# Kernel tuning notes

Hardware: AMD Instinct MI355X
Metric: run time of the kernel (lower is better)

## Reference

```python
import jax, jax.numpy as jnp
import numpy as np

F_DIMS = [16, 16, 16, 16]
F_SIZES = [16, 32, 64, 96]
HID = 128  # == 2*sum(F_DIMS)
IN_DIM = 3
OUT_DIM = 3
N = 524288
N_LAYERS = 3
N_VEC_LAYERS = 2


def sample_grid(grid, coords):
    """Trilinear grid_sample, align_corners=True, border padding.
    grid: (C, S, S, S) laid out (D, H, W); coords: (N, 3) as (x, y, z) in [-1, 1]
    where x indexes W, y indexes H, z indexes D (torch grid_sample convention).
    Returns (N, C)."""
    S = grid.shape[1]
    p = jnp.clip((coords + 1.0) * 0.5 * (S - 1), 0.0, S - 1.0)
    p0 = jnp.floor(p)
    w = p - p0
    i0 = p0.astype(jnp.int32)
    i1 = jnp.minimum(i0 + 1, S - 1)
    x0, y0, z0 = i0[:, 0], i0[:, 1], i0[:, 2]
    x1, y1, z1 = i1[:, 0], i1[:, 1], i1[:, 2]
    wx, wy, wz = w[:, 0], w[:, 1], w[:, 2]
    g = lambda z, y, x: grid[:, z, y, x]  # (C, N)
    c00 = g(z0, y0, x0) * (1 - wx) + g(z0, y0, x1) * wx
    c01 = g(z0, y1, x0) * (1 - wx) + g(z0, y1, x1) * wx
    c10 = g(z1, y0, x0) * (1 - wx) + g(z1, y0, x1) * wx
    c11 = g(z1, y1, x0) * (1 - wx) + g(z1, y1, x1) * wx
    c0 = c00 * (1 - wy) + c01 * wy
    c1 = c10 * (1 - wy) + c11 * wy
    return (c0 * (1 - wz) + c1 * wz).T  # (N, C)


def multi_level(grids, coords):
    feats = jnp.concatenate([sample_grid(g, coords) for g in grids], axis=1)
    return jax.nn.silu(feats)


def setup_inputs() -> dict:
    key = jax.random.key(0)
    ks = jax.random.split(key, 24)
    inp = {}
    inp['physical_coords'] = jax.random.normal(ks[0], (N, IN_DIM), jnp.float32)
    inp['net_coords'] = jax.random.uniform(ks[1], (N, IN_DIM), jnp.float32, -1.0, 1.0)
    inp['tau'] = jax.random.uniform(ks[2], (N, 1), jnp.float32)
    scale = 0.01
    for i, (fd, fs) in enumerate(zip(F_DIMS, F_SIZES)):
        inp[f'vec_g{i}'] = scale * jax.random.normal(ks[3 + i], (fd, fs, fs, fs), jnp.float32)
        inp[f'tau_g{i}'] = scale * jax.random.normal(ks[7 + i], (fd, fs, fs, fs), jnp.float32)
    sfd = sum(F_DIMS)  # 64

    def ffm_weight(k):
        rd = jax.random.uniform(k, (sfd, IN_DIM), jnp.float32, -1.0, 1.0)
        rd = rd / jnp.linalg.norm(rd, axis=1, keepdims=True)
        return jnp.linspace(0.5, 4.0, sfd)[:, None] * rd

    inp['vec_pe_w'] = ffm_weight(ks[11])
    inp['tau_pe_w'] = ffm_weight(ks[12])
    inp['tau_pe_b'] = jnp.zeros((sfd,), jnp.float32)
    inp['vec_scale_param'] = jnp.ones((1, HID), jnp.float32) * 0.01
    inp['vec_map_w'] = jax.random.normal(ks[13], (N_VEC_LAYERS, HID, HID), jnp.float32) / np.sqrt(HID)
    inp['tau_mlp_w'] = jax.random.normal(ks[14], (HID, HID), jnp.float32) / np.sqrt(HID)
    inp['vec_mlp_w'] = jax.random.normal(ks[15], (N_LAYERS, HID, HID), jnp.float32) / np.sqrt(HID)
    inp['tau_params'] = jnp.ones((N_LAYERS, 1, HID), jnp.float32) * 0.01
    inp['last_w'] = jax.random.normal(ks[16], (OUT_DIM, HID), jnp.float32) / np.sqrt(HID)
    return inp


def reference(physical_coords, net_coords, tau,
              vec_g0, vec_g1, vec_g2, vec_g3,
              tau_g0, tau_g1, tau_g2, tau_g3,
              vec_pe_w, tau_pe_w, tau_pe_b, vec_scale_param,
              vec_map_w, tau_mlp_w, vec_mlp_w, tau_params, last_w):
    # vector branch
    vec_grid_f = multi_level([vec_g0, vec_g1, vec_g2, vec_g3], net_coords)  # (N, 64)
    vec_ffm = jnp.sin(net_coords @ vec_pe_w.T)                               # (N, 64)
    vec_features = jnp.concatenate([vec_grid_f, vec_ffm], axis=1)           # (N, 128)
    for i in range(vec_map_w.shape[0]):
        vec_features = jax.nn.silu(vec_features @ vec_map_w[i].T)
    # tau branch
    tau_grid_f = multi_level([tau_g0, tau_g1, tau_g2, tau_g3], net_coords)
    tau_ffm = jnp.sin(net_coords @ tau_pe_w.T + tau_pe_b)
    tau_features = jnp.concatenate([tau_grid_f, tau_ffm], axis=1)           # (N, 128)
    # residual MLP stack
    out = jnp.tanh(tau * vec_scale_param * vec_features)
    for idx in range(vec_mlp_w.shape[0]):
        t_tau = jnp.tanh(tau * tau_params[idx])
        h = out @ vec_mlp_w[idx].T
        if idx == 0:
            h = h * (tau_features @ tau_mlp_w.T)
        out = out + t_tau * jax.nn.silu(h)
    return physical_coords + out @ last_w.T
```

## Files before the change

### kernel.cpp

```cpp
#include <hip/hip_runtime.h>
#include <hip/hip_bf16.h>

typedef unsigned short u16;
typedef unsigned int   u32;
typedef short bf16x8 __attribute__((ext_vector_type(8)));
typedef float f32x4  __attribute__((ext_vector_type(4)));

#define N_PTS   524288

#define WS_TAU   18939904
#define WS_MAP   37879808
#define WS_TMLP  37912576
#define WS_MLP   37928960
#define WS_TOTAL_BYTES (37978112ULL * 2ULL)

__device__ __forceinline__ void ldsfence() { __asm__ __volatile__("" ::: "memory"); }

__device__ __forceinline__ float b2f(u16 b) {
    u32 u = ((u32)b) << 16; float f; __builtin_memcpy(&f, &u, 4); return f;
}
__device__ __forceinline__ u16 f2b(float f) {
    u32 u; __builtin_memcpy(&u, &f, 4);
    u32 r = (u + 0x7FFFu + ((u >> 16) & 1u)) >> 16;
    return (u16)r;
}
__device__ __forceinline__ float frcp(float x) { return __builtin_amdgcn_rcpf(x); }
__device__ __forceinline__ float fsilu(float x) { return x * frcp(1.f + __expf(-x)); }
__device__ __forceinline__ float ftanh(float x) {
    float e = __expf(2.f * x);
    return 1.f - 2.f * frcp(e + 1.f);
}
__device__ __forceinline__ float fsin(float a) {
    return __builtin_amdgcn_sinf(a * 0.15915494309189535f);
}

__device__ __forceinline__ int aidx(int row, int ch) {
    return (row << 7) + ((((ch >> 3) ^ (row & 7))) << 3) + (ch & 7);
}

__device__ __forceinline__ void store4(u16* actw, int row, int ch,
                                       float v0, float v1, float v2, float v3) {
    u32 lo = (u32)f2b(v0) | ((u32)f2b(v1) << 16);
    u32 hi = (u32)f2b(v2) | ((u32)f2b(v3) << 16);
    *(uint2*)(actw + aidx(row, ch)) = make_uint2(lo, hi);
}

struct GridPtrs { const float* g[4]; };

struct PrepArgs {
    const float* vg[4]; const float* tg[4];
    const float* map_w; const float* tmlp; const float* mlp;
    u16* ws;
};
#define PREP_VOXB 9248
__global__ void __launch_bounds__(256) dtn_prep(PrepArgs p) {
    int b = blockIdx.x;
    if (b < PREP_VOXB) {
        int v = b * 256 + threadIdx.x;
        int set = (v >= 1183744) ? 1 : 0;
        int lv = v - set * 1183744;
        int l, base, S3, off;
        if      (lv <   4096) { l = 0; base = 0;      S3 = 4096;   off = 0;       }
        else if (lv <  36864) { l = 1; base = 4096;   S3 = 32768;  off = 65536;   }
        else if (lv < 299008) { l = 2; base = 36864;  S3 = 262144; off = 589824;  }
        else                  { l = 3; base = 299008; S3 = 884736; off = 4784128; }
        int vox = lv - base;
        const float* src = set ? p.tg[l] : p.vg[l];
        u16* dst = p.ws + (set ? WS_TAU : 0) + off + (size_t)vox * 16;
        u32 packed[8];
#pragma unroll
        for (int c = 0; c < 8; ++c) {
            u32 lo = f2b(src[(2 * c) * S3 + vox]);
            u32 hi = f2b(src[(2 * c + 1) * S3 + vox]);
            packed[c] = lo | (hi << 16);
        }
        uint4* d = (uint4*)dst;
        d[0] = make_uint4(packed[0], packed[1], packed[2], packed[3]);
        d[1] = make_uint4(packed[4], packed[5], packed[6], packed[7]);
    } else {
        int i = (b - PREP_VOXB) * 256 + threadIdx.x;
        if (i < 32768)      p.ws[WS_MAP  + i]          = f2b(p.map_w[i]);
        else if (i < 49152) p.ws[WS_TMLP + (i - 32768)] = f2b(p.tmlp[i - 32768]);
        else if (i < 98304) p.ws[WS_MLP  + (i - 49152)] = f2b(p.mlp[i - 49152]);
    }
}

template<int USE_WS, int HASB>
__device__ __forceinline__ void featurize(const u16* __restrict__ gT, GridPtrs gp,
                                          float x, float y, float z,
                                          const float* __restrict__ pe_w,
                                          const float* __restrict__ pe_b,
                                          u16* __restrict__ actw, int row)
{
    const int Ss[4]   = {16, 32, 64, 96};
    const int offs[4] = {0, 65536, 589824, 4784128};
    const int S3s[4]  = {4096, 32768, 262144, 884736};
#pragma unroll
    for (int l = 0; l < 4; ++l) {
        const int S = Ss[l];
        float fS = (float)(S - 1);
        float px = fminf(fmaxf((x + 1.f) * 0.5f * fS, 0.f), fS);
        float py = fminf(fmaxf((y + 1.f) * 0.5f * fS, 0.f), fS);
        float pz = fminf(fmaxf((z + 1.f) * 0.5f * fS, 0.f), fS);
        int ix0 = (int)px, iy0 = (int)py, iz0 = (int)pz;
        float wx = px - (float)ix0, wy = py - (float)iy0, wz = pz - (float)iz0;
        int ix1 = min(ix0 + 1, S - 1), iy1 = min(iy0 + 1, S - 1), iz1 = min(iz0 + 1, S - 1);

        float f[16];
#pragma unroll
        for (int c = 0; c < 16; ++c) f[c] = 0.f;

#pragma unroll
        for (int cz = 0; cz < 2; ++cz) {
            int zz = cz ? iz1 : iz0;
            float wgtz = cz ? wz : (1.f - wz);
#pragma unroll
            for (int cy = 0; cy < 2; ++cy) {
                int yy = cy ? iy1 : iy0;
                float wgty = wgtz * (cy ? wy : (1.f - wy));
#pragma unroll
                for (int cx = 0; cx < 2; ++cx) {
                    int xx = cx ? ix1 : ix0;
                    float wgt = wgty * (cx ? wx : (1.f - wx));
                    if (USE_WS) {
                        const u16* g = gT + offs[l];
                        const uint4* p = (const uint4*)(g + (size_t)(((zz * S) + yy) * S + xx) * 16);
                        uint4 a = p[0], b = p[1];
                        f[0]  += wgt * b2f((u16)(a.x & 0xffff));  f[1]  += wgt * b2f((u16)(a.x >> 16));
                        f[2]  += wgt * b2f((u16)(a.y & 0xffff));  f[3]  += wgt * b2f((u16)(a.y >> 16));
                        f[4]  += wgt * b2f((u16)(a.z & 0xffff));  f[5]  += wgt * b2f((u16)(a.z >> 16));
                        f[6]  += wgt * b2f((u16)(a.w & 0xffff));  f[7]  += wgt * b2f((u16)(a.w >> 16));
                        f[8]  += wgt * b2f((u16)(b.x & 0xffff));  f[9]  += wgt * b2f((u16)(b.x >> 16));
                        f[10] += wgt * b2f((u16)(b.y & 0xffff));  f[11] += wgt * b2f((u16)(b.y >> 16));
                        f[12] += wgt * b2f((u16)(b.z & 0xffff));  f[13] += wgt * b2f((u16)(b.z >> 16));
                        f[14] += wgt * b2f((u16)(b.w & 0xffff));  f[15] += wgt * b2f((u16)(b.w >> 16));
                    } else {
                        const float* gc = gp.g[l];
                        size_t vox = (size_t)((zz * S) + yy) * S + xx;
#pragma unroll
                        for (int c = 0; c < 16; ++c)
                            f[c] += wgt * gc[(size_t)c * S3s[l] + vox];
                    }
                }
            }
        }
#pragma unroll
        for (int c = 0; c < 16; c += 4)
            store4(actw, row, l * 16 + c,
                   fsilu(f[c]), fsilu(f[c + 1]), fsilu(f[c + 2]), fsilu(f[c + 3]));
    }
#pragma unroll 4
    for (int fc = 0; fc < 64; fc += 4) {
        float s[4];
#pragma unroll
        for (int j = 0; j < 4; ++j) {
            int ch = fc + j;
            float a = x * pe_w[ch * 3 + 0] + y * pe_w[ch * 3 + 1] + z * pe_w[ch * 3 + 2];
            if (HASB) a += pe_b[ch];
            s[j] = fsin(a);
        }
        store4(actw, row, 64 + fc, s[0], s[1], s[2], s[3]);
    }
}

__device__ __forceinline__ void loadB(const u16* actw, bf16x8 B[4][4], int l16, int quad) {
#pragma unroll
    for (int nt = 0; nt < 4; ++nt)
#pragma unroll
        for (int kt = 0; kt < 4; ++kt)
            B[nt][kt] = *(const bf16x8*)(actw + aidx(nt * 16 + l16, kt * 32 + quad * 8));
    ldsfence();
}

template<int USE_WS>
__device__ __forceinline__ bf16x8 loadA(const u16* WT, const float* Wf, int row, int chunk) {
    if (USE_WS) {
        return ((const bf16x8*)WT)[row * 16 + chunk];
    } else {
        const float4* p = (const float4*)(Wf + row * 128 + chunk * 8);
        float4 f0 = p[0], f1 = p[1];
        u32 w0 = (u32)f2b(f0.x) | ((u32)f2b(f0.y) << 16);
        u32 w1 = (u32)f2b(f0.z) | ((u32)f2b(f0.w) << 16);
        u32 w2 = (u32)f2b(f1.x) | ((u32)f2b(f1.y) << 16);
        u32 w3 = (u32)f2b(f1.z) | ((u32)f2b(f1.w) << 16);
        uint4 packed = make_uint4(w0, w1, w2, w3);
        bf16x8 r; __builtin_memcpy(&r, &packed, 16); return r;
    }
}

template<int USE_WS, typename Epi>
__device__ __forceinline__ void gemm128(const u16* __restrict__ WT, const float* __restrict__ Wf,
                                        const bf16x8 B[4][4],
                                        int l16, int quad, Epi&& epi)
{
#pragma unroll
    for (int mt = 0; mt < 8; ++mt) {
        f32x4 acc[4];
#pragma unroll
        for (int nt = 0; nt < 4; ++nt) acc[nt] = (f32x4){0.f, 0.f, 0.f, 0.f};
#pragma unroll
        for (int kt = 0; kt < 4; ++kt) {
            bf16x8 a = loadA<USE_WS>(WT, Wf, mt * 16 + l16, kt * 4 + quad);
#pragma unroll
            for (int nt = 0; nt < 4; ++nt)
                acc[nt] = __builtin_amdgcn_mfma_f32_16x16x32_bf16(a, B[nt][kt], acc[nt], 0, 0, 0);
        }
#pragma unroll
        for (int nt = 0; nt < 4; ++nt) epi(mt, nt, acc[nt]);
    }
}

template<int USE_WS>
__global__ void __launch_bounds__(64, 4)
dtn_main(const float* __restrict__ nc, const float* __restrict__ tauP,
         const float* __restrict__ phys, const u16* __restrict__ wsT,
         GridPtrs vgp, GridPtrs tgp,
         const float* __restrict__ vec_pe_w, const float* __restrict__ tau_pe_w,
         const float* __restrict__ tau_pe_b, const float* __restrict__ vscale,
         const float* __restrict__ map_w, const float* __restrict__ tau_mlp_w,
         const float* __restrict__ mlp_w, const float* __restrict__ tau_pars,
         const float* __restrict__ last_w, float* __restrict__ outP)
{
    __shared__ __align__(16) u16 actw[64 * 128];
    const int lane = threadIdx.x;
    const int quad = lane >> 4, l16 = lane & 15;

    const int pBase = blockIdx.x * 64;
    const int myPt  = pBase + lane;

    float cx = nc[myPt * 3 + 0];
    float cy = nc[myPt * 3 + 1];
    float cz = nc[myPt * 3 + 2];

    float tauv[4];
#pragma unroll
    for (int nt = 0; nt < 4; ++nt) tauv[nt] = tauP[pBase + nt * 16 + l16];

    const u16* wsVec = wsT;
    const u16* wsTau = wsT + WS_TAU;
    const u16* wMap  = wsT + WS_MAP;
    const u16* wTmlp = wsT + WS_TMLP;
    const u16* wMlp  = wsT + WS_MLP;

    featurize<USE_WS, 1>(wsTau, tgp, cx, cy, cz, tau_pe_w, tau_pe_b, actw, lane);
    __syncthreads();

    bf16x8 B[4][4];
    loadB(actw, B, l16, quad);
    u32 tfpPk[64];
    gemm128<USE_WS>(wTmlp, tau_mlp_w, B, l16, quad, [&](int mt, int nt, f32x4 acc) {
        int base = (mt * 4 + nt) * 2;
        tfpPk[base + 0] = (u32)f2b(acc[0]) | ((u32)f2b(acc[1]) << 16);
        tfpPk[base + 1] = (u32)f2b(acc[2]) | ((u32)f2b(acc[3]) << 16);
    });
    __syncthreads();

    featurize<USE_WS, 0>(wsVec, vgp, cx, cy, cz, vec_pe_w, (const float*)nullptr, actw, lane);
    __syncthreads();

    loadB(actw, B, l16, quad);
    gemm128<USE_WS>(wMap, map_w, B, l16, quad, [&](int mt, int nt, f32x4 acc) {
        int cb = mt * 16 + quad * 4, pt = nt * 16 + l16;
        store4(actw, pt, cb, fsilu(acc[0]), fsilu(acc[1]), fsilu(acc[2]), fsilu(acc[3]));
    });
    __syncthreads();

    loadB(actw, B, l16, quad);
    gemm128<USE_WS>(wMap + 128 * 128, map_w + 128 * 128, B, l16, quad, [&](int mt, int nt, f32x4 acc) {
        int cb = mt * 16 + quad * 4, pt = nt * 16 + l16;
        float t = tauv[nt];
        float4 vs = *(const float4*)(vscale + cb);
        store4(actw, pt, cb,
               ftanh(t * vs.x * fsilu(acc[0])), ftanh(t * vs.y * fsilu(acc[1])),
               ftanh(t * vs.z * fsilu(acc[2])), ftanh(t * vs.w * fsilu(acc[3])));
    });
    __syncthreads();

#pragma unroll
    for (int idx = 0; idx < 3; ++idx) {
        loadB(actw, B, l16, quad);
        gemm128<USE_WS>(wMlp + idx * 128 * 128, mlp_w + idx * 128 * 128, B, l16, quad,
                        [&](int mt, int nt, f32x4 acc) {
            int cb = mt * 16 + quad * 4, pt = nt * 16 + l16;
            float t = tauv[nt];
            float4 tp = *(const float4*)(tau_pars + idx * 128 + cb);
            uint2 old = *(const uint2*)(actw + aidx(pt, cb));
            float h0 = acc[0], h1 = acc[1], h2 = acc[2], h3 = acc[3];
            if (idx == 0) {
                int base = (mt * 4 + nt) * 2;
                h0 *= b2f((u16)(tfpPk[base] & 0xffff));
                h1 *= b2f((u16)(tfpPk[base] >> 16));
                h2 *= b2f((u16)(tfpPk[base + 1] & 0xffff));
                h3 *= b2f((u16)(tfpPk[base + 1] >> 16));
            }
            float n0 = b2f((u16)(old.x & 0xffff)) + ftanh(t * tp.x) * fsilu(h0);
            float n1 = b2f((u16)(old.x >> 16))    + ftanh(t * tp.y) * fsilu(h1);
            float n2 = b2f((u16)(old.y & 0xffff)) + ftanh(t * tp.z) * fsilu(h2);
            float n3 = b2f((u16)(old.y >> 16))    + ftanh(t * tp.w) * fsilu(h3);
            store4(actw, pt, cb, n0, n1, n2, n3);
        });
        __syncthreads();
    }

    float a0 = 0.f, a1 = 0.f, a2 = 0.f;
#pragma unroll
    for (int c8 = 0; c8 < 16; ++c8) {
        bf16x8 v = *(const bf16x8*)(actw + aidx(lane, c8 * 8));
        const u16* vp = (const u16*)&v;
#pragma unroll
        for (int j = 0; j < 8; ++j) {
            float av = b2f(vp[j]);
            int k = c8 * 8 + j;
            a0 += av * last_w[0 * 128 + k];
            a1 += av * last_w[1 * 128 + k];
            a2 += av * last_w[2 * 128 + k];
        }
    }
    outP[myPt * 3 + 0] = phys[myPt * 3 + 0] + a0;
    outP[myPt * 3 + 1] = phys[myPt * 3 + 1] + a1;
    outP[myPt * 3 + 2] = phys[myPt * 3 + 2] + a2;
}

extern "C" void kernel_launch(void* const* d_in, const int* in_sizes, int n_in,
                              void* d_out, int out_size, void* d_ws, size_t ws_size,
                              hipStream_t stream)
{
    const float* phys     = (const float*)d_in[0];
    const float* nc       = (const float*)d_in[1];
    const float* tau      = (const float*)d_in[2];
    GridPtrs vgp, tgp;
    bool interleaved = (in_sizes[4] == 65536);
    for (int l = 0; l < 4; ++l) {
        if (interleaved) {
            vgp.g[l] = (const float*)d_in[3 + 2 * l];
            tgp.g[l] = (const float*)d_in[4 + 2 * l];
        } else {
            vgp.g[l] = (const float*)d_in[3 + l];
            tgp.g[l] = (const float*)d_in[7 + l];
        }
    }
    const float* vec_pe_w = (const float*)d_in[11];
    const float* tau_pe_w = (const float*)d_in[12];
    const float* tau_pe_b = (const float*)d_in[13];
    const float* vscale   = (const float*)d_in[14];
    const float* map_w    = (const float*)d_in[15];
    const float* tau_mlp  = (const float*)d_in[16];
    const float* mlp_w    = (const float*)d_in[17];
    const float* tau_pars = (const float*)d_in[18];
    const float* last_w   = (const float*)d_in[19];
    u16* wsT = (u16*)d_ws;

    bool useWs = (ws_size >= WS_TOTAL_BYTES);
    if (useWs) {
        PrepArgs pa;
        for (int l = 0; l < 4; ++l) { pa.vg[l] = vgp.g[l]; pa.tg[l] = tgp.g[l]; }
        pa.map_w = map_w; pa.tmlp = tau_mlp; pa.mlp = mlp_w; pa.ws = wsT;
        dtn_prep<<<PREP_VOXB + 384, 256, 0, stream>>>(pa);
        dtn_main<1><<<N_PTS / 64, 64, 0, stream>>>(nc, tau, phys, wsT, vgp, tgp,
                                                   vec_pe_w, tau_pe_w, tau_pe_b, vscale,
                                                   map_w, tau_mlp, mlp_w, tau_pars, last_w,
                                                   (float*)d_out);
    } else {
        dtn_main<0><<<N_PTS / 64, 64, 0, stream>>>(nc, tau, phys, wsT, vgp, tgp,
                                                   vec_pe_w, tau_pe_w, tau_pe_b, vscale,
                                                   map_w, tau_mlp, mlp_w, tau_pars, last_w,
                                                   (float*)d_out);
    }
}
```

Measured before the change: 832.8 us.

## Split each 64-point block across four waves for featurize and GEMM work

The main kernel goes from one 64-thread wave per 64-point block to four waves. In featurization each wave handles one grid level and its 16 Fourier channels for all 64 points. In the GEMMs each wave owns 16 rows (points) and keeps only one N-tile of B fragments and accumulators. The last projection is split across quads and reduced with lane shuffles. The aim is to cut per-thread register pressure and serial latency by raising wave-level parallelism, at the cost of more block-level syncs and redundant weight A-fragment loads per wave.

```diff
diff --git a/kernel.cpp b/kernel.cpp
--- a/kernel.cpp
+++ b/kernel.cpp
@@ -85,72 +85,81 @@
     }
 }
 
-template<int USE_WS, int HASB>
-__device__ __forceinline__ void featurize(const u16* __restrict__ gT, GridPtrs gp,
-                                          float x, float y, float z,
-                                          const float* __restrict__ pe_w,
-                                          const float* __restrict__ pe_b,
-                                          u16* __restrict__ actw, int row)
-{
-    const int Ss[4]   = {16, 32, 64, 96};
-    const int offs[4] = {0, 65536, 589824, 4784128};
-    const int S3s[4]  = {4096, 32768, 262144, 884736};
-#pragma unroll
-    for (int l = 0; l < 4; ++l) {
-        const int S = Ss[l];
-        float fS = (float)(S - 1);
-        float px = fminf(fmaxf((x + 1.f) * 0.5f * fS, 0.f), fS);
-        float py = fminf(fmaxf((y + 1.f) * 0.5f * fS, 0.f), fS);
-        float pz = fminf(fmaxf((z + 1.f) * 0.5f * fS, 0.f), fS);
-        int ix0 = (int)px, iy0 = (int)py, iz0 = (int)pz;
-        float wx = px - (float)ix0, wy = py - (float)iy0, wz = pz - (float)iz0;
-        int ix1 = min(ix0 + 1, S - 1), iy1 = min(iy0 + 1, S - 1), iz1 = min(iz0 + 1, S - 1);
-
-        float f[16];
-#pragma unroll
-        for (int c = 0; c < 16; ++c) f[c] = 0.f;
-
-#pragma unroll
-        for (int cz = 0; cz < 2; ++cz) {
-            int zz = cz ? iz1 : iz0;
-            float wgtz = cz ? wz : (1.f - wz);
-#pragma unroll
-            for (int cy = 0; cy < 2; ++cy) {
-                int yy = cy ? iy1 : iy0;
-                float wgty = wgtz * (cy ? wy : (1.f - wy));
-#pragma unroll
-                for (int cx = 0; cx < 2; ++cx) {
-                    int xx = cx ? ix1 : ix0;
-                    float wgt = wgty * (cx ? wx : (1.f - wx));
-                    if (USE_WS) {
-                        const u16* g = gT + offs[l];
-                        const uint4* p = (const uint4*)(g + (size_t)(((zz * S) + yy) * S + xx) * 16);
-                        uint4 a = p[0], b = p[1];
-                        f[0]  += wgt * b2f((u16)(a.x & 0xffff));  f[1]  += wgt * b2f((u16)(a.x >> 16));
-                        f[2]  += wgt * b2f((u16)(a.y & 0xffff));  f[3]  += wgt * b2f((u16)(a.y >> 16));
-                        f[4]  += wgt * b2f((u16)(a.z & 0xffff));  f[5]  += wgt * b2f((u16)(a.z >> 16));
-                        f[6]  += wgt * b2f((u16)(a.w & 0xffff));  f[7]  += wgt * b2f((u16)(a.w >> 16));
-                        f[8]  += wgt * b2f((u16)(b.x & 0xffff));  f[9]  += wgt * b2f((u16)(b.x >> 16));
-                        f[10] += wgt * b2f((u16)(b.y & 0xffff));  f[11] += wgt * b2f((u16)(b.y >> 16));
-                        f[12] += wgt * b2f((u16)(b.z & 0xffff));  f[13] += wgt * b2f((u16)(b.z >> 16));
-                        f[14] += wgt * b2f((u16)(b.w & 0xffff));  f[15] += wgt * b2f((u16)(b.w >> 16));
-                    } else {
-                        const float* gc = gp.g[l];
-                        size_t vox = (size_t)((zz * S) + yy) * S + xx;
-#pragma unroll
-                        for (int c = 0; c < 16; ++c)
-                            f[c] += wgt * gc[(size_t)c * S3s[l] + vox];
-                    }
+template<int USE_WS, int LVL>
+__device__ __forceinline__ void fz_level(const u16* __restrict__ gT,
+                                         const float* __restrict__ gf,
+                                         float x, float y, float z,
+                                         u16* __restrict__ actw, int row)
+{
+    constexpr int S   = (LVL == 0) ? 16 : (LVL == 1) ? 32 : (LVL == 2) ? 64 : 96;
+    constexpr int OFF = (LVL == 0) ? 0 : (LVL == 1) ? 65536 : (LVL == 2) ? 589824 : 4784128;
+    constexpr int S3  = S * S * S;
+    const float fS = (float)(S - 1);
+    float px = fminf(fmaxf((x + 1.f) * 0.5f * fS, 0.f), fS);
+    float py = fminf(fmaxf((y + 1.f) * 0.5f * fS, 0.f), fS);
+    float pz = fminf(fmaxf((z + 1.f) * 0.5f * fS, 0.f), fS);
+    int ix0 = (int)px, iy0 = (int)py, iz0 = (int)pz;
+    float wx = px - (float)ix0, wy = py - (float)iy0, wz = pz - (float)iz0;
+    int ix1 = min(ix0 + 1, S - 1), iy1 = min(iy0 + 1, S - 1), iz1 = min(iz0 + 1, S - 1);
+
+    float f[16];
+#pragma unroll
+    for (int c = 0; c < 16; ++c) f[c] = 0.f;
+
+#pragma unroll
+    for (int cz = 0; cz < 2; ++cz) {
+        int zz = cz ? iz1 : iz0;
+        float wgtz = cz ? wz : (1.f - wz);
+#pragma unroll
+        for (int cy = 0; cy < 2; ++cy) {
+            int yy = cy ? iy1 : iy0;
+            float wgty = wgtz * (cy ? wy : (1.f - wy));
+#pragma unroll
+            for (int cx = 0; cx < 2; ++cx) {
+                int xx = cx ? ix1 : ix0;
+                float wgt = wgty * (cx ? wx : (1.f - wx));
+                if (USE_WS) {
+                    const uint4* p = (const uint4*)(gT + OFF + (size_t)(((zz * S) + yy) * S + xx) * 16);
+                    uint4 a = p[0], b = p[1];
+                    f[0]  += wgt * b2f((u16)(a.x & 0xffff));  f[1]  += wgt * b2f((u16)(a.x >> 16));
+                    f[2]  += wgt * b2f((u16)(a.y & 0xffff));  f[3]  += wgt * b2f((u16)(a.y >> 16));
+                    f[4]  += wgt * b2f((u16)(a.z & 0xffff));  f[5]  += wgt * b2f((u16)(a.z >> 16));
+                    f[6]  += wgt * b2f((u16)(a.w & 0xffff));  f[7]  += wgt * b2f((u16)(a.w >> 16));
+                    f[8]  += wgt * b2f((u16)(b.x & 0xffff));  f[9]  += wgt * b2f((u16)(b.x >> 16));
+                    f[10] += wgt * b2f((u16)(b.y & 0xffff));  f[11] += wgt * b2f((u16)(b.y >> 16));
+                    f[12] += wgt * b2f((u16)(b.z & 0xffff));  f[13] += wgt * b2f((u16)(b.z >> 16));
+                    f[14] += wgt * b2f((u16)(b.w & 0xffff));  f[15] += wgt * b2f((u16)(b.w >> 16));
+                } else {
+                    size_t vox = (size_t)((zz * S) + yy) * S + xx;
+#pragma unroll
+                    for (int c = 0; c < 16; ++c)
+                        f[c] += wgt * gf[(size_t)c * S3 + vox];
                 }
             }
         }
-#pragma unroll
-        for (int c = 0; c < 16; c += 4)
-            store4(actw, row, l * 16 + c,
-                   fsilu(f[c]), fsilu(f[c + 1]), fsilu(f[c + 2]), fsilu(f[c + 3]));
-    }
+    }
+#pragma unroll
+    for (int c = 0; c < 16; c += 4)
+        store4(actw, row, LVL * 16 + c,
+               fsilu(f[c]), fsilu(f[c + 1]), fsilu(f[c + 2]), fsilu(f[c + 3]));
+}
+
+template<int USE_WS, int HASB>
+__device__ __forceinline__ void featurize4(const u16* __restrict__ gT, GridPtrs gp, int part,
+                                           float x, float y, float z,
+                                           const float* __restrict__ pe_w,
+                                           const float* __restrict__ pe_b,
+                                           u16* __restrict__ actw, int row)
+{
+    switch (part) {
+        case 0:  fz_level<USE_WS, 0>(gT, gp.g[0], x, y, z, actw, row); break;
+        case 1:  fz_level<USE_WS, 1>(gT, gp.g[1], x, y, z, actw, row); break;
+        case 2:  fz_level<USE_WS, 2>(gT, gp.g[2], x, y, z, actw, row); break;
+        default: fz_level<USE_WS, 3>(gT, gp.g[3], x, y, z, actw, row); break;
+    }
+    const int f0 = part * 16;
 #pragma unroll 4
-    for (int fc = 0; fc < 64; fc += 4) {
+    for (int fc = f0; fc < f0 + 16; fc += 4) {
         float s[4];
 #pragma unroll
         for (int j = 0; j < 4; ++j) {
@@ -163,12 +172,10 @@
     }
 }
 
-__device__ __forceinline__ void loadB(const u16* actw, bf16x8 B[4][4], int l16, int quad) {
-#pragma unroll
-    for (int nt = 0; nt < 4; ++nt)
-#pragma unroll
-        for (int kt = 0; kt < 4; ++kt)
-            B[nt][kt] = *(const bf16x8*)(actw + aidx(nt * 16 + l16, kt * 32 + quad * 8));
+__device__ __forceinline__ void loadB(const u16* actw, bf16x8 B[4], int row, int quad) {
+#pragma unroll
+    for (int kt = 0; kt < 4; ++kt)
+        B[kt] = *(const bf16x8*)(actw + aidx(row, kt * 32 + quad * 8));
     ldsfence();
 }
 
@@ -190,28 +197,23 @@
 
 template<int USE_WS, typename Epi>
 __device__ __forceinline__ void gemm128(const u16* __restrict__ WT, const float* __restrict__ Wf,
-                                        const bf16x8 B[4][4],
+                                        const bf16x8 B[4],
                                         int l16, int quad, Epi&& epi)
 {
 #pragma unroll
     for (int mt = 0; mt < 8; ++mt) {
-        f32x4 acc[4];
-#pragma unroll
-        for (int nt = 0; nt < 4; ++nt) acc[nt] = (f32x4){0.f, 0.f, 0.f, 0.f};
+        f32x4 acc = (f32x4){0.f, 0.f, 0.f, 0.f};
 #pragma unroll
         for (int kt = 0; kt < 4; ++kt) {
             bf16x8 a = loadA<USE_WS>(WT, Wf, mt * 16 + l16, kt * 4 + quad);
-#pragma unroll
-            for (int nt = 0; nt < 4; ++nt)
-                acc[nt] = __builtin_amdgcn_mfma_f32_16x16x32_bf16(a, B[nt][kt], acc[nt], 0, 0, 0);
-        }
-#pragma unroll
-        for (int nt = 0; nt < 4; ++nt) epi(mt, nt, acc[nt]);
+            acc = __builtin_amdgcn_mfma_f32_16x16x32_bf16(a, B[kt], acc, 0, 0, 0);
+        }
+        epi(mt, acc);
     }
 }
 
 template<int USE_WS>
-__global__ void __launch_bounds__(64, 4)
+__global__ void __launch_bounds__(256, 4)
 dtn_main(const float* __restrict__ nc, const float* __restrict__ tauP,
          const float* __restrict__ phys, const u16* __restrict__ wsT,
          GridPtrs vgp, GridPtrs tgp,
@@ -222,19 +224,20 @@
          const float* __restrict__ last_w, float* __restrict__ outP)
 {
     __shared__ __align__(16) u16 actw[64 * 128];
-    const int lane = threadIdx.x;
+    const int tid  = threadIdx.x;
+    const int w    = tid >> 6;
+    const int lane = tid & 63;
     const int quad = lane >> 4, l16 = lane & 15;
+    const int row  = w * 16 + l16;
 
     const int pBase = blockIdx.x * 64;
-    const int myPt  = pBase + lane;
-
-    float cx = nc[myPt * 3 + 0];
-    float cy = nc[myPt * 3 + 1];
-    float cz = nc[myPt * 3 + 2];
-
-    float tauv[4];
-#pragma unroll
-    for (int nt = 0; nt < 4; ++nt) tauv[nt] = tauP[pBase + nt * 16 + l16];
+    const int fzPt  = pBase + lane;
+    const int myPt  = pBase + row;
+
+    float cx = nc[fzPt * 3 + 0];
+    float cy = nc[fzPt * 3 + 1];
+    float cz = nc[fzPt * 3 + 2];
+    float tauv = tauP[myPt];
 
     const u16* wsVec = wsT;
     const u16* wsTau = wsT + WS_TAU;
@@ -242,83 +245,85 @@
     const u16* wTmlp = wsT + WS_TMLP;
     const u16* wMlp  = wsT + WS_MLP;
 
-    featurize<USE_WS, 1>(wsTau, tgp, cx, cy, cz, tau_pe_w, tau_pe_b, actw, lane);
-    __syncthreads();
-
-    bf16x8 B[4][4];
-    loadB(actw, B, l16, quad);
-    u32 tfpPk[64];
-    gemm128<USE_WS>(wTmlp, tau_mlp_w, B, l16, quad, [&](int mt, int nt, f32x4 acc) {
-        int base = (mt * 4 + nt) * 2;
-        tfpPk[base + 0] = (u32)f2b(acc[0]) | ((u32)f2b(acc[1]) << 16);
-        tfpPk[base + 1] = (u32)f2b(acc[2]) | ((u32)f2b(acc[3]) << 16);
+    featurize4<USE_WS, 1>(wsTau, tgp, w, cx, cy, cz, tau_pe_w, tau_pe_b, actw, lane);
+    __syncthreads();
+
+    bf16x8 B[4];
+    loadB(actw, B, row, quad);
+    u32 tfpPk[16];
+    gemm128<USE_WS>(wTmlp, tau_mlp_w, B, l16, quad, [&](int mt, f32x4 acc) {
+        tfpPk[mt * 2 + 0] = (u32)f2b(acc[0]) | ((u32)f2b(acc[1]) << 16);
+        tfpPk[mt * 2 + 1] = (u32)f2b(acc[2]) | ((u32)f2b(acc[3]) << 16);
     });
     __syncthreads();
 
-    featurize<USE_WS, 0>(wsVec, vgp, cx, cy, cz, vec_pe_w, (const float*)nullptr, actw, lane);
-    __syncthreads();
-
-    loadB(actw, B, l16, quad);
-    gemm128<USE_WS>(wMap, map_w, B, l16, quad, [&](int mt, int nt, f32x4 acc) {
-        int cb = mt * 16 + quad * 4, pt = nt * 16 + l16;
-        store4(actw, pt, cb, fsilu(acc[0]), fsilu(acc[1]), fsilu(acc[2]), fsilu(acc[3]));
+    featurize4<USE_WS, 0>(wsVec, vgp, w, cx, cy, cz, vec_pe_w, (const float*)nullptr, actw, lane);
+    __syncthreads();
+
+    loadB(actw, B, row, quad);
+    gemm128<USE_WS>(wMap, map_w, B, l16, quad, [&](int mt, f32x4 acc) {
+        int cb = mt * 16 + quad * 4;
+        store4(actw, row, cb, fsilu(acc[0]), fsilu(acc[1]), fsilu(acc[2]), fsilu(acc[3]));
     });
     __syncthreads();
 
-    loadB(actw, B, l16, quad);
-    gemm128<USE_WS>(wMap + 128 * 128, map_w + 128 * 128, B, l16, quad, [&](int mt, int nt, f32x4 acc) {
-        int cb = mt * 16 + quad * 4, pt = nt * 16 + l16;
-        float t = tauv[nt];
+    loadB(actw, B, row, quad);
+    gemm128<USE_WS>(wMap + 128 * 128, map_w + 128 * 128, B, l16, quad, [&](int mt, f32x4 acc) {
+        int cb = mt * 16 + quad * 4;
         float4 vs = *(const float4*)(vscale + cb);
-        store4(actw, pt, cb,
-               ftanh(t * vs.x * fsilu(acc[0])), ftanh(t * vs.y * fsilu(acc[1])),
-               ftanh(t * vs.z * fsilu(acc[2])), ftanh(t * vs.w * fsilu(acc[3])));
+        store4(actw, row, cb,
+               ftanh(tauv * vs.x * fsilu(acc[0])), ftanh(tauv * vs.y * fsilu(acc[1])),
+               ftanh(tauv * vs.z * fsilu(acc[2])), ftanh(tauv * vs.w * fsilu(acc[3])));
     });
     __syncthreads();
 
 #pragma unroll
     for (int idx = 0; idx < 3; ++idx) {
-        loadB(actw, B, l16, quad);
+        loadB(actw, B, row, quad);
         gemm128<USE_WS>(wMlp + idx * 128 * 128, mlp_w + idx * 128 * 128, B, l16, quad,
-                        [&](int mt, int nt, f32x4 acc) {
-            int cb = mt * 16 + quad * 4, pt = nt * 16 + l16;
-            float t = tauv[nt];
+                        [&](int mt, f32x4 acc) {
+            int cb = mt * 16 + quad * 4;
             float4 tp = *(const float4*)(tau_pars + idx * 128 + cb);
-            uint2 old = *(const uint2*)(actw + aidx(pt, cb));
+            uint2 old = *(const uint2*)(actw + aidx(row, cb));
             float h0 = acc[0], h1 = acc[1], h2 = acc[2], h3 = acc[3];
             if (idx == 0) {
-                int base = (mt * 4 + nt) * 2;
-                h0 *= b2f((u16)(tfpPk[base] & 0xffff));
-                h1 *= b2f((u16)(tfpPk[base] >> 16));
-                h2 *= b2f((u16)(tfpPk[base + 1] & 0xffff));
-                h3 *= b2f((u16)(tfpPk[base + 1] >> 16));
+                h0 *= b2f((u16)(tfpPk[mt * 2] & 0xffff));
+                h1 *= b2f((u16)(tfpPk[mt * 2] >> 16));
+                h2 *= b2f((u16)(tfpPk[mt * 2 + 1] & 0xffff));
+                h3 *= b2f((u16)(tfpPk[mt * 2 + 1] >> 16));
             }
-            float n0 = b2f((u16)(old.x & 0xffff)) + ftanh(t * tp.x) * fsilu(h0);
-            float n1 = b2f((u16)(old.x >> 16))    + ftanh(t * tp.y) * fsilu(h1);
-            float n2 = b2f((u16)(old.y & 0xffff)) + ftanh(t * tp.z) * fsilu(h2);
-            float n3 = b2f((u16)(old.y >> 16))    + ftanh(t * tp.w) * fsilu(h3);
-            store4(actw, pt, cb, n0, n1, n2, n3);
+            float n0 = b2f((u16)(old.x & 0xffff)) + ftanh(tauv * tp.x) * fsilu(h0);
+            float n1 = b2f((u16)(old.x >> 16))    + ftanh(tauv * tp.y) * fsilu(h1);
+            float n2 = b2f((u16)(old.y & 0xffff)) + ftanh(tauv * tp.z) * fsilu(h2);
+            float n3 = b2f((u16)(old.y >> 16))    + ftanh(tauv * tp.w) * fsilu(h3);
+            store4(actw, row, cb, n0, n1, n2, n3);
         });
         __syncthreads();
     }
 
     float a0 = 0.f, a1 = 0.f, a2 = 0.f;
 #pragma unroll
-    for (int c8 = 0; c8 < 16; ++c8) {
-        bf16x8 v = *(const bf16x8*)(actw + aidx(lane, c8 * 8));
+    for (int c8 = 0; c8 < 4; ++c8) {
+        int kb = quad * 32 + c8 * 8;
+        bf16x8 v = *(const bf16x8*)(actw + aidx(row, kb));
         const u16* vp = (const u16*)&v;
 #pragma unroll
         for (int j = 0; j < 8; ++j) {
             float av = b2f(vp[j]);
-            int k = c8 * 8 + j;
+            int k = kb + j;
             a0 += av * last_w[0 * 128 + k];
             a1 += av * last_w[1 * 128 + k];
             a2 += av * last_w[2 * 128 + k];
         }
     }
-    outP[myPt * 3 + 0] = phys[myPt * 3 + 0] + a0;
-    outP[myPt * 3 + 1] = phys[myPt * 3 + 1] + a1;
-    outP[myPt * 3 + 2] = phys[myPt * 3 + 2] + a2;
+    a0 += __shfl_xor(a0, 16); a0 += __shfl_xor(a0, 32);
+    a1 += __shfl_xor(a1, 16); a1 += __shfl_xor(a1, 32);
+    a2 += __shfl_xor(a2, 16); a2 += __shfl_xor(a2, 32);
+    if (quad == 0) {
+        outP[myPt * 3 + 0] = phys[myPt * 3 + 0] + a0;
+        outP[myPt * 3 + 1] = phys[myPt * 3 + 1] + a1;
+        outP[myPt * 3 + 2] = phys[myPt * 3 + 2] + a2;
+    }
 }
 
 extern "C" void kernel_launch(void* const* d_in, const int* in_sizes, int n_in,
@@ -356,14 +361,14 @@
         for (int l = 0; l < 4; ++l) { pa.vg[l] = vgp.g[l]; pa.tg[l] = tgp.g[l]; }
         pa.map_w = map_w; pa.tmlp = tau_mlp; pa.mlp = mlp_w; pa.ws = wsT;
         dtn_prep<<<PREP_VOXB + 384, 256, 0, stream>>>(pa);
-        dtn_main<1><<<N_PTS / 64, 64, 0, stream>>>(nc, tau, phys, wsT, vgp, tgp,
-                                                   vec_pe_w, tau_pe_w, tau_pe_b, vscale,
-                                                   map_w, tau_mlp, mlp_w, tau_pars, last_w,
-                                                   (float*)d_out);
+        dtn_main<1><<<N_PTS / 64, 256, 0, stream>>>(nc, tau, phys, wsT, vgp, tgp,
+                                                    vec_pe_w, tau_pe_w, tau_pe_b, vscale,
+                                                    map_w, tau_mlp, mlp_w, tau_pars, last_w,
+                                                    (float*)d_out);
     } else {
-        dtn_main<0><<<N_PTS / 64, 64, 0, stream>>>(nc, tau, phys, wsT, vgp, tgp,
-                                                   vec_pe_w, tau_pe_w, tau_pe_b, vscale,
-                                                   map_w, tau_mlp, mlp_w, tau_pars, last_w,
-                                                   (float*)d_out);
-    }
-}
+        dtn_main<0><<<N_PTS / 64, 256, 0, stream>>>(nc, tau, phys, wsT, vgp, tgp,
+                                                    vec_pe_w, tau_pe_w, tau_pe_b, vscale,
+                                                    map_w, tau_mlp, mlp_w, tau_pars, last_w,
+                                                    (float*)d_out);
+    }
+}
```

New measurement: 1.282 ms. +54.0%, slower.

## Split each point's featurization across two lanes, halving points per block

Applied to the files above, without the earlier changes.

Each 64-lane block now handles 32 points instead of 64. Two lanes share a point: each does two grid levels and half the Fourier features, and the final projection is reduced with a cross-half shuffle. The GEMM tiles shrink to two N-tiles, which cuts register use (tfpPk, B fragments, accumulators), and launch_bounds drops the minimum-occupancy hint. The aim is more parallelism and occupancy for the latency-bound gather phase, at the cost of twice as many blocks and each block reloading the weight matrices for half as many points.

```diff
diff --git a/kernel.cpp b/kernel.cpp
--- a/kernel.cpp
+++ b/kernel.cpp
@@ -86,25 +86,28 @@
 }
 
 template<int USE_WS, int HASB>
-__device__ __forceinline__ void featurize(const u16* __restrict__ gT, GridPtrs gp,
-                                          float x, float y, float z,
-                                          const float* __restrict__ pe_w,
-                                          const float* __restrict__ pe_b,
-                                          u16* __restrict__ actw, int row)
+__device__ __forceinline__ void featurize32(const u16* __restrict__ gT, GridPtrs gp, int h,
+                                            float x, float y, float z,
+                                            const float* __restrict__ pe_w,
+                                            const float* __restrict__ pe_b,
+                                            u16* __restrict__ actw, int row)
 {
-    const int Ss[4]   = {16, 32, 64, 96};
-    const int offs[4] = {0, 65536, 589824, 4784128};
-    const int S3s[4]  = {4096, 32768, 262144, 884736};
-#pragma unroll
-    for (int l = 0; l < 4; ++l) {
-        const int S = Ss[l];
-        float fS = (float)(S - 1);
+#pragma unroll
+    for (int lv2 = 0; lv2 < 2; ++lv2) {
+        const int l = h * 2 + lv2;
+        const int S   = (l == 0) ? 16 : (l == 1) ? 32 : (l == 2) ? 64 : 96;
+        const int OFF = (l == 0) ? 0  : (l == 1) ? 65536 : (l == 2) ? 589824 : 4784128;
+        const float fS = (float)(S - 1);
         float px = fminf(fmaxf((x + 1.f) * 0.5f * fS, 0.f), fS);
         float py = fminf(fmaxf((y + 1.f) * 0.5f * fS, 0.f), fS);
         float pz = fminf(fmaxf((z + 1.f) * 0.5f * fS, 0.f), fS);
         int ix0 = (int)px, iy0 = (int)py, iz0 = (int)pz;
         float wx = px - (float)ix0, wy = py - (float)iy0, wz = pz - (float)iz0;
         int ix1 = min(ix0 + 1, S - 1), iy1 = min(iy0 + 1, S - 1), iz1 = min(iz0 + 1, S - 1);
+        int dx = ix1 - ix0;
+        int dy = (iy1 - iy0) * S;
+        int dz = (iz1 - iz0) * S * S;
+        int i000 = (iz0 * S + iy0) * S + ix0;
 
         float f[16];
 #pragma unroll
@@ -112,19 +115,18 @@
 
 #pragma unroll
         for (int cz = 0; cz < 2; ++cz) {
-            int zz = cz ? iz1 : iz0;
             float wgtz = cz ? wz : (1.f - wz);
+            int iz = cz ? dz : 0;
 #pragma unroll
             for (int cy = 0; cy < 2; ++cy) {
-                int yy = cy ? iy1 : iy0;
                 float wgty = wgtz * (cy ? wy : (1.f - wy));
+                int izy = iz + (cy ? dy : 0);
 #pragma unroll
                 for (int cx = 0; cx < 2; ++cx) {
-                    int xx = cx ? ix1 : ix0;
                     float wgt = wgty * (cx ? wx : (1.f - wx));
+                    int idx = i000 + izy + (cx ? dx : 0);
                     if (USE_WS) {
-                        const u16* g = gT + offs[l];
-                        const uint4* p = (const uint4*)(g + (size_t)(((zz * S) + yy) * S + xx) * 16);
+                        const uint4* p = (const uint4*)(gT + OFF + (size_t)idx * 16);
                         uint4 a = p[0], b = p[1];
                         f[0]  += wgt * b2f((u16)(a.x & 0xffff));  f[1]  += wgt * b2f((u16)(a.x >> 16));
                         f[2]  += wgt * b2f((u16)(a.y & 0xffff));  f[3]  += wgt * b2f((u16)(a.y >> 16));
@@ -135,11 +137,12 @@
                         f[12] += wgt * b2f((u16)(b.z & 0xffff));  f[13] += wgt * b2f((u16)(b.z >> 16));
                         f[14] += wgt * b2f((u16)(b.w & 0xffff));  f[15] += wgt * b2f((u16)(b.w >> 16));
                     } else {
-                        const float* gc = gp.g[l];
-                        size_t vox = (size_t)((zz * S) + yy) * S + xx;
+                        const float* gf = (l == 0) ? gp.g[0] : (l == 1) ? gp.g[1]
+                                        : (l == 2) ? gp.g[2] : gp.g[3];
+                        const int S3 = S * S * S;
 #pragma unroll
                         for (int c = 0; c < 16; ++c)
-                            f[c] += wgt * gc[(size_t)c * S3s[l] + vox];
+                            f[c] += wgt * gf[(size_t)c * S3 + idx];
                     }
                 }
             }
@@ -149,23 +152,24 @@
             store4(actw, row, l * 16 + c,
                    fsilu(f[c]), fsilu(f[c + 1]), fsilu(f[c + 2]), fsilu(f[c + 3]));
     }
+    const int f0 = h * 32;
 #pragma unroll 4
-    for (int fc = 0; fc < 64; fc += 4) {
+    for (int fc = 0; fc < 32; fc += 4) {
         float s[4];
 #pragma unroll
         for (int j = 0; j < 4; ++j) {
-            int ch = fc + j;
+            int ch = f0 + fc + j;
             float a = x * pe_w[ch * 3 + 0] + y * pe_w[ch * 3 + 1] + z * pe_w[ch * 3 + 2];
             if (HASB) a += pe_b[ch];
             s[j] = fsin(a);
         }
-        store4(actw, row, 64 + fc, s[0], s[1], s[2], s[3]);
-    }
-}
-
-__device__ __forceinline__ void loadB(const u16* actw, bf16x8 B[4][4], int l16, int quad) {
-#pragma unroll
-    for (int nt = 0; nt < 4; ++nt)
+        store4(actw, row, 64 + f0 + fc, s[0], s[1], s[2], s[3]);
+    }
+}
+
+__device__ __forceinline__ void loadB(const u16* actw, bf16x8 B[2][4], int l16, int quad) {
+#pragma unroll
+    for (int nt = 0; nt < 2; ++nt)
 #pragma unroll
         for (int kt = 0; kt < 4; ++kt)
             B[nt][kt] = *(const bf16x8*)(actw + aidx(nt * 16 + l16, kt * 32 + quad * 8));
@@ -190,28 +194,28 @@
 
 template<int USE_WS, typename Epi>
 __device__ __forceinline__ void gemm128(const u16* __restrict__ WT, const float* __restrict__ Wf,
-                                        const bf16x8 B[4][4],
+                                        const bf16x8 B[2][4],
                                         int l16, int quad, Epi&& epi)
 {
-#pragma unroll
+#pragma unroll 2
     for (int mt = 0; mt < 8; ++mt) {
-        f32x4 acc[4];
-#pragma unroll
-        for (int nt = 0; nt < 4; ++nt) acc[nt] = (f32x4){0.f, 0.f, 0.f, 0.f};
+        f32x4 acc[2];
+#pragma unroll
+        for (int nt = 0; nt < 2; ++nt) acc[nt] = (f32x4){0.f, 0.f, 0.f, 0.f};
 #pragma unroll
         for (int kt = 0; kt < 4; ++kt) {
             bf16x8 a = loadA<USE_WS>(WT, Wf, mt * 16 + l16, kt * 4 + quad);
 #pragma unroll
-            for (int nt = 0; nt < 4; ++nt)
+            for (int nt = 0; nt < 2; ++nt)
                 acc[nt] = __builtin_amdgcn_mfma_f32_16x16x32_bf16(a, B[nt][kt], acc[nt], 0, 0, 0);
         }
 #pragma unroll
-        for (int nt = 0; nt < 4; ++nt) epi(mt, nt, acc[nt]);
+        for (int nt = 0; nt < 2; ++nt) epi(mt, nt, acc[nt]);
     }
 }
 
 template<int USE_WS>
-__global__ void __launch_bounds__(64, 4)
+__global__ void __launch_bounds__(64)
 dtn_main(const float* __restrict__ nc, const float* __restrict__ tauP,
          const float* __restrict__ phys, const u16* __restrict__ wsT,
          GridPtrs vgp, GridPtrs tgp,
@@ -221,20 +225,22 @@
          const float* __restrict__ mlp_w, const float* __restrict__ tau_pars,
          const float* __restrict__ last_w, float* __restrict__ outP)
 {
-    __shared__ __align__(16) u16 actw[64 * 128];
+    __shared__ __align__(16) u16 actw[32 * 128];
     const int lane = threadIdx.x;
+    const int h    = lane >> 5;
+    const int pt   = lane & 31;
     const int quad = lane >> 4, l16 = lane & 15;
 
-    const int pBase = blockIdx.x * 64;
-    const int myPt  = pBase + lane;
-
-    float cx = nc[myPt * 3 + 0];
-    float cy = nc[myPt * 3 + 1];
-    float cz = nc[myPt * 3 + 2];
-
-    float tauv[4];
-#pragma unroll
-    for (int nt = 0; nt < 4; ++nt) tauv[nt] = tauP[pBase + nt * 16 + l16];
+    const int pBase = blockIdx.x * 32;
+    const int fzPt  = pBase + pt;
+
+    float cx = nc[fzPt * 3 + 0];
+    float cy = nc[fzPt * 3 + 1];
+    float cz = nc[fzPt * 3 + 2];
+
+    float tauv[2];
+#pragma unroll
+    for (int nt = 0; nt < 2; ++nt) tauv[nt] = tauP[pBase + nt * 16 + l16];
 
     const u16* wsVec = wsT;
     const u16* wsTau = wsT + WS_TAU;
@@ -242,35 +248,35 @@
     const u16* wTmlp = wsT + WS_TMLP;
     const u16* wMlp  = wsT + WS_MLP;
 
-    featurize<USE_WS, 1>(wsTau, tgp, cx, cy, cz, tau_pe_w, tau_pe_b, actw, lane);
-    __syncthreads();
-
-    bf16x8 B[4][4];
+    featurize32<USE_WS, 1>(wsTau, tgp, h, cx, cy, cz, tau_pe_w, tau_pe_b, actw, pt);
+    __syncthreads();
+
+    bf16x8 B[2][4];
     loadB(actw, B, l16, quad);
-    u32 tfpPk[64];
+    u32 tfpPk[32];
     gemm128<USE_WS>(wTmlp, tau_mlp_w, B, l16, quad, [&](int mt, int nt, f32x4 acc) {
-        int base = (mt * 4 + nt) * 2;
+        int base = (mt * 2 + nt) * 2;
         tfpPk[base + 0] = (u32)f2b(acc[0]) | ((u32)f2b(acc[1]) << 16);
         tfpPk[base + 1] = (u32)f2b(acc[2]) | ((u32)f2b(acc[3]) << 16);
     });
     __syncthreads();
 
-    featurize<USE_WS, 0>(wsVec, vgp, cx, cy, cz, vec_pe_w, (const float*)nullptr, actw, lane);
+    featurize32<USE_WS, 0>(wsVec, vgp, h, cx, cy, cz, vec_pe_w, (const float*)nullptr, actw, pt);
     __syncthreads();
 
     loadB(actw, B, l16, quad);
     gemm128<USE_WS>(wMap, map_w, B, l16, quad, [&](int mt, int nt, f32x4 acc) {
-        int cb = mt * 16 + quad * 4, pt = nt * 16 + l16;
-        store4(actw, pt, cb, fsilu(acc[0]), fsilu(acc[1]), fsilu(acc[2]), fsilu(acc[3]));
+        int cb = mt * 16 + quad * 4, prow = nt * 16 + l16;
+        store4(actw, prow, cb, fsilu(acc[0]), fsilu(acc[1]), fsilu(acc[2]), fsilu(acc[3]));
     });
     __syncthreads();
 
     loadB(actw, B, l16, quad);
     gemm128<USE_WS>(wMap + 128 * 128, map_w + 128 * 128, B, l16, quad, [&](int mt, int nt, f32x4 acc) {
-        int cb = mt * 16 + quad * 4, pt = nt * 16 + l16;
+        int cb = mt * 16 + quad * 4, prow = nt * 16 + l16;
         float t = tauv[nt];
         float4 vs = *(const float4*)(vscale + cb);
-        store4(actw, pt, cb,
+        store4(actw, prow, cb,
                ftanh(t * vs.x * fsilu(acc[0])), ftanh(t * vs.y * fsilu(acc[1])),
                ftanh(t * vs.z * fsilu(acc[2])), ftanh(t * vs.w * fsilu(acc[3])));
     });
@@ -281,13 +287,13 @@
         loadB(actw, B, l16, quad);
         gemm128<USE_WS>(wMlp + idx * 128 * 128, mlp_w + idx * 128 * 128, B, l16, quad,
                         [&](int mt, int nt, f32x4 acc) {
-            int cb = mt * 16 + quad * 4, pt = nt * 16 + l16;
+            int cb = mt * 16 + quad * 4, prow = nt * 16 + l16;
             float t = tauv[nt];
             float4 tp = *(const float4*)(tau_pars + idx * 128 + cb);
-            uint2 old = *(const uint2*)(actw + aidx(pt, cb));
+            uint2 old = *(const uint2*)(actw + aidx(prow, cb));
             float h0 = acc[0], h1 = acc[1], h2 = acc[2], h3 = acc[3];
             if (idx == 0) {
-                int base = (mt * 4 + nt) * 2;
+                int base = (mt * 2 + nt) * 2;
                 h0 *= b2f((u16)(tfpPk[base] & 0xffff));
                 h1 *= b2f((u16)(tfpPk[base] >> 16));
                 h2 *= b2f((u16)(tfpPk[base + 1] & 0xffff));
@@ -297,28 +303,34 @@
             float n1 = b2f((u16)(old.x >> 16))    + ftanh(t * tp.y) * fsilu(h1);
             float n2 = b2f((u16)(old.y & 0xffff)) + ftanh(t * tp.z) * fsilu(h2);
             float n3 = b2f((u16)(old.y >> 16))    + ftanh(t * tp.w) * fsilu(h3);
-            store4(actw, pt, cb, n0, n1, n2, n3);
+            store4(actw, prow, cb, n0, n1, n2, n3);
         });
         __syncthreads();
     }
 
     float a0 = 0.f, a1 = 0.f, a2 = 0.f;
 #pragma unroll
-    for (int c8 = 0; c8 < 16; ++c8) {
-        bf16x8 v = *(const bf16x8*)(actw + aidx(lane, c8 * 8));
+    for (int c8 = 0; c8 < 8; ++c8) {
+        int kb = h * 64 + c8 * 8;
+        bf16x8 v = *(const bf16x8*)(actw + aidx(pt, kb));
         const u16* vp = (const u16*)&v;
 #pragma unroll
         for (int j = 0; j < 8; ++j) {
             float av = b2f(vp[j]);
-            int k = c8 * 8 + j;
+            int k = kb + j;
             a0 += av * last_w[0 * 128 + k];
             a1 += av * last_w[1 * 128 + k];
             a2 += av * last_w[2 * 128 + k];
         }
     }
-    outP[myPt * 3 + 0] = phys[myPt * 3 + 0] + a0;
-    outP[myPt * 3 + 1] = phys[myPt * 3 + 1] + a1;
-    outP[myPt * 3 + 2] = phys[myPt * 3 + 2] + a2;
+    a0 += __shfl_xor(a0, 32);
+    a1 += __shfl_xor(a1, 32);
+    a2 += __shfl_xor(a2, 32);
+    if (h == 0) {
+        outP[fzPt * 3 + 0] = phys[fzPt * 3 + 0] + a0;
+        outP[fzPt * 3 + 1] = phys[fzPt * 3 + 1] + a1;
+        outP[fzPt * 3 + 2] = phys[fzPt * 3 + 2] + a2;
+    }
 }
 
 extern "C" void kernel_launch(void* const* d_in, const int* in_sizes, int n_in,
@@ -356,12 +368,12 @@
         for (int l = 0; l < 4; ++l) { pa.vg[l] = vgp.g[l]; pa.tg[l] = tgp.g[l]; }
         pa.map_w = map_w; pa.tmlp = tau_mlp; pa.mlp = mlp_w; pa.ws = wsT;
         dtn_prep<<<PREP_VOXB + 384, 256, 0, stream>>>(pa);
-        dtn_main<1><<<N_PTS / 64, 64, 0, stream>>>(nc, tau, phys, wsT, vgp, tgp,
+        dtn_main<1><<<N_PTS / 32, 64, 0, stream>>>(nc, tau, phys, wsT, vgp, tgp,
                                                    vec_pe_w, tau_pe_w, tau_pe_b, vscale,
                                                    map_w, tau_mlp, mlp_w, tau_pars, last_w,
                                                    (float*)d_out);
     } else {
-        dtn_main<0><<<N_PTS / 64, 64, 0, stream>>>(nc, tau, phys, wsT, vgp, tgp,
+        dtn_main<0><<<N_PTS / 32, 64, 0, stream>>>(nc, tau, phys, wsT, vgp, tgp,
                                                    vec_pe_w, tau_pe_w, tau_pe_b, vscale,
                                                    map_w, tau_mlp, mlp_w, tau_pars, last_w,
                                                    (float*)d_out);
```

Result: faster. 791.3 us (-5.0%).
